# Performance work log

Measured on AMD Instinct MI355X. Metric: run time of the kernel, lower is better.

## Reference

```python
import jax, jax.numpy as jnp
import numpy as np

B, T, D, H = 4, 2048, 1024, 16
HD = D // H  # head dim = 64

def setup_inputs() -> dict:
    key = jax.random.key(0)
    ks = jax.random.split(key, 4)
    scale = 1.0 / np.sqrt(D)
    return {
        "hidden_states": jax.random.normal(ks[0], (B, T, D), dtype=jnp.float32),
        "attention_mask": jnp.zeros((B, 1, 1, T), dtype=jnp.float32),
        "Wq": jax.random.normal(ks[1], (D, D), dtype=jnp.float32) * scale,
        "bq": jnp.zeros((D,), dtype=jnp.float32),
        "Wk": jax.random.normal(ks[2], (D, D), dtype=jnp.float32) * scale,
        "bk": jnp.zeros((D,), dtype=jnp.float32),
        "Wv": jax.random.normal(ks[3], (D, D), dtype=jnp.float32) * scale,
        "bv": jnp.zeros((D,), dtype=jnp.float32),
    }

def _split_heads(x):
    # [B, T, D] -> [B, H, T, HD]
    b, t, _ = x.shape
    return x.reshape(b, t, H, HD).transpose(0, 2, 1, 3)

def reference(hidden_states, attention_mask, Wq, bq, Wk, bk, Wv, bv):
    q = _split_heads(hidden_states @ Wq.T + bq)
    k = _split_heads(hidden_states @ Wk.T + bk)
    v = _split_heads(hidden_states @ Wv.T + bv)
    # scores: [B, H, T, T]
    scores = jnp.einsum("bhqd,bhkd->bhqk", q, k) * (HD ** -0.5)
    t = hidden_states.shape[1]
    causal = jnp.triu(jnp.ones((t, t), dtype=bool), k=1)  # True above diagonal -> masked
    scores = jnp.where(causal[None, None], -jnp.inf, scores)
    scores = scores + attention_mask  # additive padding mask [B,1,1,T]
    probs = jax.nn.softmax(scores, axis=-1)
    out = jnp.einsum("bhqk,bhkd->bhqd", probs, v)
    # [B, H, T, HD] -> [B, T, D]
    return out.transpose(0, 2, 1, 3).reshape(hidden_states.shape[0], t, D)
```

## Files before the change

kernel.cpp:

```cpp
#include <hip/hip_runtime.h>
#include <hip/hip_bf16.h>
#include <stdint.h>

#define TT 2048
#define DD 1024
#define HH 16
#define HDIM 64
#define BB 4
#define MROWS 8192
#define LOG2E 1.44269504088896340736f

typedef __attribute__((ext_vector_type(8))) short short8;
typedef __attribute__((ext_vector_type(4))) float floatx4;

__device__ __forceinline__ ushort f2bf(float f){
  uint32_t u = __builtin_bit_cast(uint32_t, f);
  u = u + 0x7fffu + ((u >> 16) & 1u);
  return (ushort)(u >> 16);
}
__device__ __forceinline__ float bf2f(ushort s){
  uint32_t u = ((uint32_t)s) << 16;
  return __builtin_bit_cast(float, u);
}

__device__ __forceinline__ uint32_t cvtpk(float lo, float hi){
  uint32_t r;
  asm("v_cvt_pk_bf16_f32 %0, %1, %2" : "=v"(r) : "v"(lo), "v"(hi));
  return r;
}

__device__ __forceinline__ float exp2a(float x){
  float r;
  asm("v_exp_f32 %0, %1" : "=v"(r) : "v"(x));
  return r;
}

__device__ __forceinline__ void gld16(const void* g, void* l){
  __builtin_amdgcn_global_load_lds((const __attribute__((address_space(1))) uint32_t*)g,
                                   (__attribute__((address_space(3))) uint32_t*)l, 16, 0, 0);
}

__global__ void cvt_bf16(const float* __restrict__ src, ushort* __restrict__ dst, int n4){
  int i = blockIdx.x*blockDim.x + threadIdx.x;
  if (i < n4){
    float4 v = ((const float4*)src)[i];
    ushort4 o;
    o.x = f2bf(v.x); o.y = f2bf(v.y); o.z = f2bf(v.z); o.w = f2bf(v.w);
    ((ushort4*)dst)[i] = o;
  }
}

__global__ void cvt_w3(const float* __restrict__ wq, const float* __restrict__ wk,
                       const float* __restrict__ wv, ushort* __restrict__ dst){
  int m = blockIdx.y;
  const float* s = (m==0)? wq : (m==1? wk : wv);
  int i = blockIdx.x*blockDim.x + threadIdx.x;
  float4 v = ((const float4*)s)[i];
  ushort4 o;
  o.x = f2bf(v.x); o.y = f2bf(v.y); o.z = f2bf(v.z); o.w = f2bf(v.w);
  ((ushort4*)(dst + (size_t)m*DD*DD))[i] = o;
}

__global__ void w2_prep(const float* __restrict__ am, ushort* __restrict__ w2){
  int i = blockIdx.x*blockDim.x + threadIdx.x;
  if (i < BB*TT) w2[i] = f2bf(__expf(am[i]));
}

__global__ __launch_bounds__(256) void qkv_gemm(
    const ushort* __restrict__ A, const ushort* __restrict__ Wall,
    const float* __restrict__ bq, const float* __restrict__ bk, const float* __restrict__ bv,
    const ushort* __restrict__ w2,
    ushort* __restrict__ Qo, ushort* __restrict__ Ko, ushort* __restrict__ Vo)
{
  __shared__ __align__(16) ushort sA[2][128*64];
  __shared__ __align__(16) ushort sB[2][128*64];
  const int mat = blockIdx.z;
  const ushort* W = Wall + (size_t)mat*DD*DD;
  const float* bias = (mat==0)? bq : (mat==1? bk : bv);
  ushort* out = (mat==0)? Qo : (mat==1? Ko : Vo);
  const float oscale = (mat==0)? 0.125f*LOG2E : 1.0f;
  const bool matV = (mat == 2);
  const int m0 = blockIdx.x*128, n0 = blockIdx.y*128;
  const int tid = threadIdx.x, lane = tid & 63, wid = tid >> 6;
  const int wm = (wid>>1)*64, wn = (wid&1)*64;
  const int c = lane & 15, g = lane >> 4;
  const int srow = lane >> 3;
  const int scol = ((lane & 7) ^ srow) * 8;

  floatx4 acc[4][4];
  #pragma unroll
  for (int i=0;i<4;i++)
    #pragma unroll
    for(int j=0;j<4;j++) acc[i][j] = (floatx4){0.f,0.f,0.f,0.f};

  auto stage = [&](int k0, int buf){
    #pragma unroll
    for (int j=0;j<4;j++){
      int chunk = wid*4 + j;
      int row = chunk*8 + srow;
      gld16(A + (size_t)(m0+row)*DD + k0 + scol, sA[buf] + chunk*512);
      gld16(W + (size_t)(n0+row)*DD + k0 + scol, sB[buf] + chunk*512);
    }
  };

  const int rsw = (c & 7) * 8;

  stage(0, 0);
  for (int kt = 0; kt < 16; ++kt){
    if (kt+1 < 16){
      stage((kt+1)*64, (kt+1)&1);
      asm volatile("s_waitcnt vmcnt(8)" ::: "memory");
    } else {
      asm volatile("s_waitcnt vmcnt(0)" ::: "memory");
    }
    __builtin_amdgcn_s_barrier();
    __builtin_amdgcn_sched_barrier(0);

    const ushort* cA = sA[kt&1];
    const ushort* cB = sB[kt&1];
    #pragma unroll
    for (int ch=0; ch<2; ++ch){
      short8 af[4], bfr[4];
      #pragma unroll
      for (int mf=0; mf<4; ++mf)
        af[mf] = *(const short8*)(cA + (wm + mf*16 + c)*64 + ((ch*32 + g*8) ^ rsw));
      #pragma unroll
      for (int nf=0; nf<4; ++nf)
        bfr[nf] = *(const short8*)(cB + (wn + nf*16 + c)*64 + ((ch*32 + g*8) ^ rsw));
      if (matV){
        #pragma unroll
        for (int mf=0; mf<4; ++mf)
          #pragma unroll
          for (int nf=0; nf<4; ++nf)
            acc[mf][nf] = __builtin_amdgcn_mfma_f32_16x16x32_bf16(af[mf], bfr[nf], acc[mf][nf], 0,0,0);
      } else {
        #pragma unroll
        for (int mf=0; mf<4; ++mf)
          #pragma unroll
          for (int nf=0; nf<4; ++nf)
            acc[mf][nf] = __builtin_amdgcn_mfma_f32_16x16x32_bf16(bfr[nf], af[mf], acc[mf][nf], 0,0,0);
      }
    }
    __builtin_amdgcn_sched_barrier(0);
    __builtin_amdgcn_s_barrier();
  }

  if (matV){
    #pragma unroll
    for (int nf=0; nf<4; ++nf){
      int col = n0 + wn + nf*16 + c;
      float bval = bias[col];
      int h = col >> 6, hd = col & 63;
      #pragma unroll
      for (int mf=0; mf<4; ++mf){
        int rowb = m0 + wm + mf*16 + g*4;
        int b = rowb >> 11, t = rowb & (TT-1);
        ushort4 wv = *(const ushort4*)(w2 + (size_t)b*TT + t);
        ushort4 st;
        st.x = f2bf((acc[mf][nf][0] + bval) * bf2f(wv.x));
        st.y = f2bf((acc[mf][nf][1] + bval) * bf2f(wv.y));
        st.z = f2bf((acc[mf][nf][2] + bval) * bf2f(wv.z));
        st.w = f2bf((acc[mf][nf][3] + bval) * bf2f(wv.w));
        *(ushort4*)(out + ((size_t)(b*HH + h)*HDIM + hd)*TT + t) = st;
      }
    }
  } else {
    #pragma unroll
    for (int nf=0; nf<4; ++nf){
      int feat = n0 + wn + nf*16 + g*4;
      float4 b4 = *(const float4*)(bias + feat);
      int h = feat >> 6, hd = feat & 63;
      #pragma unroll
      for (int mf=0; mf<4; ++mf){
        int trow = m0 + wm + mf*16 + c;
        int b = trow >> 11, t = trow & (TT-1);
        ushort4 st;
        st.x = f2bf((acc[mf][nf][0] + b4.x) * oscale);
        st.y = f2bf((acc[mf][nf][1] + b4.y) * oscale);
        st.z = f2bf((acc[mf][nf][2] + b4.z) * oscale);
        st.w = f2bf((acc[mf][nf][3] + b4.w) * oscale);
        *(ushort4*)(out + ((size_t)(b*HH + h)*TT + t)*HDIM + hd) = st;
      }
    }
  }
}

__global__ __launch_bounds__(256,3) void attn_fwd(
    const ushort* __restrict__ Q, const ushort* __restrict__ K, const ushort* __restrict__ VT,
    const ushort* __restrict__ W2, float* __restrict__ O)
{
  __shared__ __align__(16) ushort sKt[2][4096];
  __shared__ __align__(16) ushort sVt[2][4096];
  __shared__ __align__(16) uint32_t sP[4][256];

  const int bh = blockIdx.x, b = bh >> 4, h = bh & 15;
  const int pr = blockIdx.y;
  const int qt1 = pr, qt2 = 31 - pr;
  const int nt1 = qt1 + 1;
  const int ntot = qt1 + qt2 + 2;
  const int tid = threadIdx.x, lane = tid & 63, w = tid >> 6;
  const int c = lane & 15, g = lane >> 4;
  uint32_t* sPw = sP[w];

  const char* Kbh = (const char*)(K  + (size_t)bh*TT*HDIM);
  const char* Vbh = (const char*)(VT + (size_t)bh*HDIM*TT);
  const ushort* w2b = W2 + (size_t)b*TT;

  auto stage = [&](int f){
    int it = (f >= nt1) ? f - nt1 : f;
    int kv0 = it*64;
    int buf = f & 1;
    int rlo = w*8 + (lane>>3);
    int colb = (lane & 7)*16;
    #pragma unroll
    for (int j=0;j<2;++j){
      int row = j*32 + rlo;
      int sw = (row & 7) << 4;
      gld16(Kbh + (size_t)(kv0+row)*128 + (colb ^ sw), &sKt[buf][j*2048 + w*512]);
      gld16(Vbh + (size_t)row*(TT*2) + (size_t)kv0*2 + (colb ^ sw), &sVt[buf][j*2048 + w*512]);
    }
  };

  short8 qf[2];
  floatx4 oacc[4], lacc;
  float mreg;
  int qmy = qt1*64 + w*16 + c;

  auto loadq = [&](int qt_){
    qmy = qt_*64 + w*16 + c;
    #pragma unroll
    for (int ch=0; ch<2; ++ch)
      qf[ch] = *(const short8*)(Q + ((size_t)bh*TT + qmy)*HDIM + ch*32 + g*8);
  };
  auto reset_state = [&](){
    mreg = -1e30f;
    lacc = (floatx4){0.f,0.f,0.f,0.f};
    #pragma unroll
    for (int d=0; d<4; ++d) oacc[d] = (floatx4){0.f,0.f,0.f,0.f};
  };
  auto writeout = [&](){
    float rl = 1.f / lacc[0];
    #pragma unroll
    for (int d=0; d<4; ++d){
      float4 st;
      st.x = oacc[d][0]*rl; st.y = oacc[d][1]*rl;
      st.z = oacc[d][2]*rl; st.w = oacc[d][3]*rl;
      *(float4*)(O + ((size_t)b*TT + qmy)*DD + h*HDIM + d*16 + g*4) = st;
    }
  };

  loadq(qt1);
  reset_state();
  stage(0);

  int qt = qt1;
  for (int f=0; f<ntot; ++f){
    if (f == nt1){
      writeout();
      reset_state();
      loadq(qt2);
      qt = qt2;
    }
    const int it = (f >= nt1) ? f - nt1 : f;
    const int kv0 = it*64;

    short8 wfr[2];
    wfr[0] = *(const short8*)(w2b + kv0 + g*8);
    wfr[1] = *(const short8*)(w2b + kv0 + 32 + g*8);
    if (f+1 < ntot){
      stage(f+1);
      asm volatile("s_waitcnt vmcnt(4)" ::: "memory");
    } else {
      asm volatile("s_waitcnt vmcnt(0)" ::: "memory");
    }
    __builtin_amdgcn_s_barrier();
    __builtin_amdgcn_sched_barrier(0);

    const ushort* bK = sKt[f&1];
    const ushort* bV = sVt[f&1];
    const int rsw = (c & 7) << 3;

    short8 kf[2][4];
    #pragma unroll
    for (int ch=0; ch<2; ++ch)
      #pragma unroll
      for (int nt=0; nt<4; ++nt)
        kf[ch][nt] = *(const short8*)(bK + (nt*16 + c)*64 + ((ch*32 + g*8) ^ rsw));

    floatx4 sacc[4];
    #pragma unroll
    for (int i=0;i<4;i++) sacc[i] = (floatx4){0.f,0.f,0.f,0.f};
    __builtin_amdgcn_s_setprio(1);
    #pragma unroll
    for (int ch=0; ch<2; ++ch)
      #pragma unroll
      for (int nt=0; nt<4; ++nt)
        sacc[nt] = __builtin_amdgcn_mfma_f32_16x16x32_bf16(kf[ch][nt], qf[ch], sacc[nt], 0,0,0);
    __builtin_amdgcn_s_setprio(0);

    float p[4][4];
    float mx = -1e30f;
    if (it == qt){
      #pragma unroll
      for (int nt=0; nt<4; ++nt)
        #pragma unroll
        for (int r=0; r<4; ++r){
          int kv = kv0 + nt*16 + g*4 + r;
          float s = (kv > qmy) ? -1e30f : sacc[nt][r];
          p[nt][r] = s;
          mx = fmaxf(mx, s);
        }
    } else {
      #pragma unroll
      for (int nt=0; nt<4; ++nt)
        #pragma unroll
        for (int r=0; r<4; ++r){
          p[nt][r] = sacc[nt][r];
          mx = fmaxf(mx, sacc[nt][r]);
        }
    }
    mx = fmaxf(mx, __shfl_xor(mx, 16));
    mx = fmaxf(mx, __shfl_xor(mx, 32));
    if (!__all(mx <= mreg + 8.f)){
      float mn = fmaxf(mreg, mx);
      float sc = exp2a(mreg - mn);
      mreg = mn;
      lacc *= sc;
      #pragma unroll
      for (int d=0; d<4; ++d)
        #pragma unroll
        for (int r=0; r<4; ++r) oacc[d][r] *= sc;
    }
    #pragma unroll
    for (int nt=0; nt<4; ++nt)
      #pragma unroll
      for (int r=0; r<4; ++r)
        p[nt][r] = exp2a(p[nt][r] - mreg);

    short8 pbr[2];
    #pragma unroll
    for (int half=0; half<2; ++half){
      #pragma unroll
      for (int nt2=0; nt2<2; ++nt2){
        int nt = half*2 + nt2;
        int dl = c + 16*(nt2*2 + (g>>1));
        uint2 pk;
        pk.x = cvtpk(p[nt][0], p[nt][1]);
        pk.y = cvtpk(p[nt][2], p[nt][3]);
        *(uint2*)(sPw + dl*4 + (g&1)*2) = pk;
      }
      pbr[half] = *(const short8*)((const ushort*)sPw + lane*8);
    }

    short8 vf[2][4];
    #pragma unroll
    for (int ch=0; ch<2; ++ch)
      #pragma unroll
      for (int d=0; d<4; ++d)
        vf[ch][d] = *(const short8*)(bV + (d*16 + c)*64 + ((ch*32 + g*8) ^ rsw));
    __builtin_amdgcn_s_setprio(1);
    #pragma unroll
    for (int d=0; d<4; ++d)
      #pragma unroll
      for (int ch=0; ch<2; ++ch)
        oacc[d] = __builtin_amdgcn_mfma_f32_16x16x32_bf16(vf[ch][d], pbr[ch], oacc[d], 0,0,0);
    #pragma unroll
    for (int ch=0; ch<2; ++ch)
      lacc = __builtin_amdgcn_mfma_f32_16x16x32_bf16(wfr[ch], pbr[ch], lacc, 0,0,0);
    __builtin_amdgcn_s_setprio(0);

    __builtin_amdgcn_sched_barrier(0);
    __builtin_amdgcn_s_barrier();
  }
  writeout();
}

extern "C" void kernel_launch(void* const* d_in, const int* in_sizes, int n_in,
                              void* d_out, int out_size, void* d_ws, size_t ws_size,
                              hipStream_t stream){
  const float* hs    = (const float*)d_in[0];
  const float* amask = (const float*)d_in[1];
  const float* Wq    = (const float*)d_in[2];
  const float* bq    = (const float*)d_in[3];
  const float* Wk    = (const float*)d_in[4];
  const float* bk    = (const float*)d_in[5];
  const float* Wv    = (const float*)d_in[6];
  const float* bv    = (const float*)d_in[7];
  float* out = (float*)d_out;

  ushort* hsb = (ushort*)d_ws;
  ushort* wb  = hsb + (size_t)MROWS*DD;
  ushort* qb  = wb  + (size_t)3*DD*DD;
  ushort* kb  = qb  + (size_t)MROWS*DD;
  ushort* vtb = kb  + (size_t)MROWS*DD;
  ushort* w2b = vtb + (size_t)MROWS*DD;

  cvt_bf16<<<(MROWS*DD/4)/256, 256, 0, stream>>>(hs, hsb, MROWS*DD/4);
  cvt_w3<<<dim3((DD*DD/4)/256, 3), 256, 0, stream>>>(Wq, Wk, Wv, wb);
  w2_prep<<<(BB*TT)/256, 256, 0, stream>>>(amask, w2b);

  qkv_gemm<<<dim3(MROWS/128, DD/128, 3), 256, 0, stream>>>(hsb, wb, bq, bk, bv, w2b, qb, kb, vtb);
  attn_fwd<<<dim3(64, 16), 256, 0, stream>>>(qb, kb, vtb, w2b, out);
}
```

Measured before the change: 151.8 us.

## Process two query tiles per block with triple-buffered KV and LDS mask

Each attention block now handles 128 query rows (two 64-row groups), so every loaded K/V tile is reused across both groups, halving K/V traffic per query row. The K/V staging becomes a three-deep ring prefetched two tiles ahead, which removes the trailing barrier of each iteration. The mask weights move into LDS once per block. The cost is more registers and LDS per block, so occupancy drops to 2 blocks per CU, and the grid is halved.

```diff
diff --git a/kernel.cpp b/kernel.cpp
--- a/kernel.cpp
+++ b/kernel.cpp
@@ -185,22 +185,22 @@
   }
 }
 
-__global__ __launch_bounds__(256,3) void attn_fwd(
+__global__ __launch_bounds__(256,2) void attn_fwd(
     const ushort* __restrict__ Q, const ushort* __restrict__ K, const ushort* __restrict__ VT,
     const ushort* __restrict__ W2, float* __restrict__ O)
 {
-  __shared__ __align__(16) ushort sKt[2][4096];
-  __shared__ __align__(16) ushort sVt[2][4096];
-  __shared__ __align__(16) uint32_t sP[4][256];
+  __shared__ __align__(16) ushort sKt[3][4096];
+  __shared__ __align__(16) ushort sVt[3][4096];
+  __shared__ __align__(16) ushort sW2[TT];
+  __shared__ __align__(16) uint32_t sP[4][2][256];
 
   const int bh = blockIdx.x, b = bh >> 4, h = bh & 15;
   const int pr = blockIdx.y;
-  const int qt1 = pr, qt2 = 31 - pr;
-  const int nt1 = qt1 + 1;
-  const int ntot = qt1 + qt2 + 2;
+  const int qt1 = pr, qt2 = 15 - pr;
+  const int nt1 = 2*qt1 + 2;
+  const int ntot = 34;
   const int tid = threadIdx.x, lane = tid & 63, w = tid >> 6;
   const int c = lane & 15, g = lane >> 4;
-  uint32_t* sPw = sP[w];
 
   const char* Kbh = (const char*)(K  + (size_t)bh*TT*HDIM);
   const char* Vbh = (const char*)(VT + (size_t)bh*HDIM*TT);
@@ -209,7 +209,7 @@
   auto stage = [&](int f){
     int it = (f >= nt1) ? f - nt1 : f;
     int kv0 = it*64;
-    int buf = f & 1;
+    int buf = f % 3;
     int rlo = w*8 + (lane>>3);
     int colb = (lane & 7)*16;
     #pragma unroll
@@ -221,42 +221,53 @@
     }
   };
 
-  short8 qf[2];
-  floatx4 oacc[4], lacc;
-  float mreg;
-  int qmy = qt1*64 + w*16 + c;
-
+  short8 qf[2][2];
   auto loadq = [&](int qt_){
-    qmy = qt_*64 + w*16 + c;
-    #pragma unroll
-    for (int ch=0; ch<2; ++ch)
-      qf[ch] = *(const short8*)(Q + ((size_t)bh*TT + qmy)*HDIM + ch*32 + g*8);
+    #pragma unroll
+    for (int grp=0; grp<2; ++grp){
+      int qmy = qt_*128 + grp*64 + w*16 + c;
+      #pragma unroll
+      for (int ch=0; ch<2; ++ch)
+        qf[grp][ch] = *(const short8*)(Q + ((size_t)bh*TT + qmy)*HDIM + ch*32 + g*8);
+    }
   };
+
+  floatx4 oacc[2][4], lacc[2];
+  float mreg[2];
   auto reset_state = [&](){
-    mreg = -1e30f;
-    lacc = (floatx4){0.f,0.f,0.f,0.f};
-    #pragma unroll
-    for (int d=0; d<4; ++d) oacc[d] = (floatx4){0.f,0.f,0.f,0.f};
+    #pragma unroll
+    for (int grp=0; grp<2; ++grp){
+      mreg[grp] = -1e30f;
+      lacc[grp] = (floatx4){0.f,0.f,0.f,0.f};
+      #pragma unroll
+      for (int d=0; d<4; ++d) oacc[grp][d] = (floatx4){0.f,0.f,0.f,0.f};
+    }
   };
-  auto writeout = [&](){
-    float rl = 1.f / lacc[0];
-    #pragma unroll
-    for (int d=0; d<4; ++d){
-      float4 st;
-      st.x = oacc[d][0]*rl; st.y = oacc[d][1]*rl;
-      st.z = oacc[d][2]*rl; st.w = oacc[d][3]*rl;
-      *(float4*)(O + ((size_t)b*TT + qmy)*DD + h*HDIM + d*16 + g*4) = st;
+  auto writeout = [&](int qt_){
+    #pragma unroll
+    for (int grp=0; grp<2; ++grp){
+      int qmy = qt_*128 + grp*64 + w*16 + c;
+      float rl = 1.f / lacc[grp][0];
+      #pragma unroll
+      for (int d=0; d<4; ++d){
+        float4 st;
+        st.x = oacc[grp][d][0]*rl; st.y = oacc[grp][d][1]*rl;
+        st.z = oacc[grp][d][2]*rl; st.w = oacc[grp][d][3]*rl;
+        *(float4*)(O + ((size_t)b*TT + qmy)*DD + h*HDIM + d*16 + g*4) = st;
+      }
     }
   };
 
+  gld16(w2b + w*512 + lane*8, sW2 + w*512);
   loadq(qt1);
   reset_state();
   stage(0);
+  stage(1);
 
   int qt = qt1;
   for (int f=0; f<ntot; ++f){
     if (f == nt1){
-      writeout();
+      writeout(qt1);
       reset_state();
       loadq(qt2);
       qt = qt2;
@@ -264,21 +275,19 @@
     const int it = (f >= nt1) ? f - nt1 : f;
     const int kv0 = it*64;
 
-    short8 wfr[2];
-    wfr[0] = *(const short8*)(w2b + kv0 + g*8);
-    wfr[1] = *(const short8*)(w2b + kv0 + 32 + g*8);
-    if (f+1 < ntot){
-      stage(f+1);
-      asm volatile("s_waitcnt vmcnt(4)" ::: "memory");
-    } else {
-      asm volatile("s_waitcnt vmcnt(0)" ::: "memory");
-    }
+    if (f < ntot-1) asm volatile("s_waitcnt vmcnt(4)" ::: "memory");
+    else            asm volatile("s_waitcnt vmcnt(0)" ::: "memory");
     __builtin_amdgcn_s_barrier();
     __builtin_amdgcn_sched_barrier(0);
-
-    const ushort* bK = sKt[f&1];
-    const ushort* bV = sVt[f&1];
+    if (f+2 < ntot) stage(f+2);
+
+    const ushort* bK = sKt[f%3];
+    const ushort* bV = sVt[f%3];
     const int rsw = (c & 7) << 3;
+
+    short8 wfr[2];
+    wfr[0] = *(const short8*)(sW2 + kv0 + g*8);
+    wfr[1] = *(const short8*)(sW2 + kv0 + 32 + g*8);
 
     short8 kf[2][4];
     #pragma unroll
@@ -287,69 +296,75 @@
       for (int nt=0; nt<4; ++nt)
         kf[ch][nt] = *(const short8*)(bK + (nt*16 + c)*64 + ((ch*32 + g*8) ^ rsw));
 
-    floatx4 sacc[4];
-    #pragma unroll
-    for (int i=0;i<4;i++) sacc[i] = (floatx4){0.f,0.f,0.f,0.f};
-    __builtin_amdgcn_s_setprio(1);
-    #pragma unroll
-    for (int ch=0; ch<2; ++ch)
+    short8 pbr[2][2];
+    #pragma unroll
+    for (int grp=0; grp<2; ++grp){
+      if (grp==0 && it > 2*qt) continue;
+      const int qmy = qt*128 + grp*64 + w*16 + c;
+      floatx4 sacc[4];
+      #pragma unroll
+      for (int i=0;i<4;i++) sacc[i] = (floatx4){0.f,0.f,0.f,0.f};
+      __builtin_amdgcn_s_setprio(1);
+      #pragma unroll
+      for (int ch=0; ch<2; ++ch)
+        #pragma unroll
+        for (int nt=0; nt<4; ++nt)
+          sacc[nt] = __builtin_amdgcn_mfma_f32_16x16x32_bf16(kf[ch][nt], qf[grp][ch], sacc[nt], 0,0,0);
+      __builtin_amdgcn_s_setprio(0);
+
+      float p[4][4];
+      float mx = -1e30f;
+      if (it == 2*qt + grp){
+        #pragma unroll
+        for (int nt=0; nt<4; ++nt)
+          #pragma unroll
+          for (int r=0; r<4; ++r){
+            int kv = kv0 + nt*16 + g*4 + r;
+            float s = (kv > qmy) ? -1e30f : sacc[nt][r];
+            p[nt][r] = s;
+            mx = fmaxf(mx, s);
+          }
+      } else {
+        #pragma unroll
+        for (int nt=0; nt<4; ++nt)
+          #pragma unroll
+          for (int r=0; r<4; ++r){
+            p[nt][r] = sacc[nt][r];
+            mx = fmaxf(mx, sacc[nt][r]);
+          }
+      }
+      mx = fmaxf(mx, __shfl_xor(mx, 16));
+      mx = fmaxf(mx, __shfl_xor(mx, 32));
+      if (!__all(mx <= mreg[grp] + 8.f)){
+        float mn = fmaxf(mreg[grp], mx);
+        float sc = exp2a(mreg[grp] - mn);
+        mreg[grp] = mn;
+        lacc[grp] *= sc;
+        #pragma unroll
+        for (int d=0; d<4; ++d)
+          #pragma unroll
+          for (int r=0; r<4; ++r) oacc[grp][d][r] *= sc;
+      }
       #pragma unroll
       for (int nt=0; nt<4; ++nt)
-        sacc[nt] = __builtin_amdgcn_mfma_f32_16x16x32_bf16(kf[ch][nt], qf[ch], sacc[nt], 0,0,0);
-    __builtin_amdgcn_s_setprio(0);
-
-    float p[4][4];
-    float mx = -1e30f;
-    if (it == qt){
-      #pragma unroll
-      for (int nt=0; nt<4; ++nt)
-        #pragma unroll
-        for (int r=0; r<4; ++r){
-          int kv = kv0 + nt*16 + g*4 + r;
-          float s = (kv > qmy) ? -1e30f : sacc[nt][r];
-          p[nt][r] = s;
-          mx = fmaxf(mx, s);
+        #pragma unroll
+        for (int r=0; r<4; ++r)
+          p[nt][r] = exp2a(p[nt][r] - mreg[grp]);
+
+      uint32_t* sPw = sP[w][grp];
+      #pragma unroll
+      for (int half=0; half<2; ++half){
+        #pragma unroll
+        for (int nt2=0; nt2<2; ++nt2){
+          int nt = half*2 + nt2;
+          int dl = c + 16*(nt2*2 + (g>>1));
+          uint2 pk;
+          pk.x = cvtpk(p[nt][0], p[nt][1]);
+          pk.y = cvtpk(p[nt][2], p[nt][3]);
+          *(uint2*)(sPw + dl*4 + (g&1)*2) = pk;
         }
-    } else {
-      #pragma unroll
-      for (int nt=0; nt<4; ++nt)
-        #pragma unroll
-        for (int r=0; r<4; ++r){
-          p[nt][r] = sacc[nt][r];
-          mx = fmaxf(mx, sacc[nt][r]);
-        }
-    }
-    mx = fmaxf(mx, __shfl_xor(mx, 16));
-    mx = fmaxf(mx, __shfl_xor(mx, 32));
-    if (!__all(mx <= mreg + 8.f)){
-      float mn = fmaxf(mreg, mx);
-      float sc = exp2a(mreg - mn);
-      mreg = mn;
-      lacc *= sc;
-      #pragma unroll
-      for (int d=0; d<4; ++d)
-        #pragma unroll
-        for (int r=0; r<4; ++r) oacc[d][r] *= sc;
-    }
-    #pragma unroll
-    for (int nt=0; nt<4; ++nt)
-      #pragma unroll
-      for (int r=0; r<4; ++r)
-        p[nt][r] = exp2a(p[nt][r] - mreg);
-
-    short8 pbr[2];
-    #pragma unroll
-    for (int half=0; half<2; ++half){
-      #pragma unroll
-      for (int nt2=0; nt2<2; ++nt2){
-        int nt = half*2 + nt2;
-        int dl = c + 16*(nt2*2 + (g>>1));
-        uint2 pk;
-        pk.x = cvtpk(p[nt][0], p[nt][1]);
-        pk.y = cvtpk(p[nt][2], p[nt][3]);
-        *(uint2*)(sPw + dl*4 + (g&1)*2) = pk;
-      }
-      pbr[half] = *(const short8*)((const ushort*)sPw + lane*8);
+        pbr[grp][half] = *(const short8*)((const ushort*)sPw + lane*8);
+      }
     }
 
     short8 vf[2][4];
@@ -360,19 +375,20 @@
         vf[ch][d] = *(const short8*)(bV + (d*16 + c)*64 + ((ch*32 + g*8) ^ rsw));
     __builtin_amdgcn_s_setprio(1);
     #pragma unroll
-    for (int d=0; d<4; ++d)
+    for (int grp=0; grp<2; ++grp){
+      if (grp==0 && it > 2*qt) continue;
+      #pragma unroll
+      for (int d=0; d<4; ++d)
+        #pragma unroll
+        for (int ch=0; ch<2; ++ch)
+          oacc[grp][d] = __builtin_amdgcn_mfma_f32_16x16x32_bf16(vf[ch][d], pbr[grp][ch], oacc[grp][d], 0,0,0);
       #pragma unroll
       for (int ch=0; ch<2; ++ch)
-        oacc[d] = __builtin_amdgcn_mfma_f32_16x16x32_bf16(vf[ch][d], pbr[ch], oacc[d], 0,0,0);
-    #pragma unroll
-    for (int ch=0; ch<2; ++ch)
-      lacc = __builtin_amdgcn_mfma_f32_16x16x32_bf16(wfr[ch], pbr[ch], lacc, 0,0,0);
+        lacc[grp] = __builtin_amdgcn_mfma_f32_16x16x32_bf16(wfr[ch], pbr[grp][ch], lacc[grp], 0,0,0);
+    }
     __builtin_amdgcn_s_setprio(0);
-
-    __builtin_amdgcn_sched_barrier(0);
-    __builtin_amdgcn_s_barrier();
   }
-  writeout();
+  writeout(qt2);
 }
 
 extern "C" void kernel_launch(void* const* d_in, const int* in_sizes, int n_in,
@@ -400,5 +416,5 @@
   w2_prep<<<(BB*TT)/256, 256, 0, stream>>>(amask, w2b);
 
   qkv_gemm<<<dim3(MROWS/128, DD/128, 3), 256, 0, stream>>>(hsb, wb, bq, bk, bv, w2b, qb, kb, vtb);
-  attn_fwd<<<dim3(64, 16), 256, 0, stream>>>(qb, kb, vtb, w2b, out);
-}
+  attn_fwd<<<dim3(64, 8), 256, 0, stream>>>(qb, kb, vtb, w2b, out);
+}
```

After: 152.4 us. No clear change (+0.4%).
